# Performance work log

Measured on AMD Instinct MI355X. Metric: run time of the kernel, lower is better.

Reference implementation:

```python
import jax, jax.numpy as jnp
import numpy as np

B, C, H, W = 8, 3, 512, 512
KH = KW = 17          # blur kernel
F_REG, D = 24, 4      # regularization filters, Wiener filters
RKH = RKW = 5         # reg-filter kernel size


def psf2otf(psf, shape):
    """Zero-pad psf to `shape`, circshift so center is at (0,0), FFT."""
    kh, kw = psf.shape[-2:]
    Ho, Wo = shape
    pad = [(0, 0)] * (psf.ndim - 2) + [(0, Ho - kh), (0, Wo - kw)]
    p = jnp.pad(psf, pad)
    p = jnp.roll(p, (-(kh // 2), -(kw // 2)), axis=(-2, -1))
    return jnp.fft.fft2(p)


def edgetaper(img, psf):
    """MATLAB-style edgetaper. img: (C,Hp,Wp), psf: (kh,kw)."""
    Ho, Wo = img.shape[-2:]

    def autocorr(proj, n):
        z = jnp.zeros((n,), img.dtype).at[: proj.shape[0]].set(proj)
        z = jnp.fft.ifft(jnp.abs(jnp.fft.fft(z)) ** 2).real
        z = jnp.concatenate([z, z[:1]])  # length n+1
        return z / z.max()

    beta0 = autocorr(psf.sum(1), Ho - 1)  # (Ho,)
    beta1 = autocorr(psf.sum(0), Wo - 1)  # (Wo,)
    alpha = (1.0 - beta0)[:, None] * (1.0 - beta1)[None, :]  # (Ho,Wo)
    blurred = jnp.fft.ifft2(jnp.fft.fft2(img) * psf2otf(psf, (Ho, Wo))).real
    return alpha * img + (1.0 - alpha) * blurred


def wiener_one(y, psf, g, log_alpha):
    """Multi-filter Wiener deconvolution for one image.
    y: (C,Hp,Wp), psf: (kh,kw), g: (F,1,rkh,rkw), log_alpha: (D,1).
    Returns (D,C,Hp,Wp)."""
    Ho, Wo = y.shape[-2:]
    K = psf2otf(psf, (Ho, Wo))                  # (Hp,Wp) complex
    G = psf2otf(g[:, 0], (Ho, Wo))              # (F,Hp,Wp)
    Greg = jnp.sum(jnp.abs(G) ** 2, axis=0)     # (Hp,Wp)
    Y = jnp.fft.fft2(y)                         # (C,Hp,Wp)
    a = jnp.exp(log_alpha)[:, :, None, None]    # (D,1,1,1)
    S = jnp.abs(K) ** 2 + a * Greg              # (D,1,Hp,Wp)
    X = (jnp.conj(K) * Y)[None] / S             # (D,C,Hp,Wp)
    return jnp.fft.ifft2(X).real


def forward(image, blurKernel, stdn, wiener_conv_weights, wiener_scale, alpha, weights):
    kh, kw = blurKernel.shape[-2:]
    # getPad2RetainShape
    pt, pb = (kh + 1) // 2 - 1, kh - (kh + 1) // 2
    pl, pr = (kw + 1) // 2 - 1, kw - (kw + 1) // 2
    x = jnp.pad(image, ((0, 0), (0, 0), (pt, pb), (pl, pr)), mode='symmetric')
    psf = blurKernel[:, 0]                      # (B,kh,kw)
    x = jax.vmap(edgetaper)(x, psf)             # (B,C,Hp,Wp)
    # WeightNormalization: zero-mean then L2-normalize per filter, times scale
    w = wiener_conv_weights - wiener_conv_weights.mean(axis=(1, 2, 3), keepdims=True)
    nrm = jnp.sqrt(jnp.sum(w * w, axis=(1, 2, 3), keepdims=True))
    w = w * (wiener_scale.reshape(-1, 1, 1, 1) / nrm)
    xw = jax.vmap(lambda yi, ki: wiener_one(yi, ki, w, alpha))(x, psf)  # (B,D,C,Hp,Wp)
    Hp, Wp = x.shape[-2:]
    crop = xw[..., pt:Hp - pb, pl:Wp - pr]      # Crop2D back to (H,W)
    return jnp.sum(crop * weights, axis=1)      # weighted mix over D -> (B,C,H,W)


def setup_inputs() -> dict:
    key = jax.random.key(0)
    ks = jax.random.split(key, 4)
    image = jax.random.uniform(ks[0], (B, C, H, W), jnp.float32)
    k = jax.random.uniform(ks[1], (B, 1, KH, KW), jnp.float32)
    blurKernel = k / jnp.sum(k, axis=(-2, -1), keepdims=True)  # normalized psf
    stdn = jax.random.uniform(ks[2], (B,), jnp.float32) * 0.05 + 0.01
    wiener_conv_weights = jax.random.normal(ks[3], (F_REG, 1, RKH, RKW), jnp.float32)
    wiener_scale = jnp.full((F_REG,), 0.1, jnp.float32)
    alpha = jnp.log(jnp.logspace(np.log10(1e-3), np.log10(1e-1), D))[:, None].astype(jnp.float32)
    weights = jnp.full((1, D, 1, 1, 1), 1.0 / D, jnp.float32)
    return {"image": image, "blurKernel": blurKernel, "stdn": stdn,
            "wiener_conv_weights": wiener_conv_weights, "wiener_scale": wiener_scale,
            "alpha": alpha, "weights": weights}


def reference(image, blurKernel, stdn, wiener_conv_weights, wiener_scale, alpha, weights):
    return forward(image, blurKernel, stdn, wiener_conv_weights, wiener_scale, alpha, weights)
```

## Files before the change

### kernel.cpp

```cpp
#include <hip/hip_runtime.h>
#include <hip/hip_bf16.h>

#define NN 528
#define NP (NN*NN)
#define IMG 512
#define IMGP (IMG*IMG)
#define PAD 8
#define KH 17
#define KT (KH*KH)
#define NF 24
#define RK 5
#define RKT (RK*RK)
#define ND 4
#define TOPB (17*NN)
#define ROWB (2*TOPB)
#define SIDEB (494*34)
#define BORD (ROWB + SIDEB)

static __device__ __forceinline__ float ldx(const void* p, long i, int bf) {
    if (bf) return __bfloat162float(((const __hip_bfloat16*)p)[i]);
    return ((const float*)p)[i];
}

static __device__ __forceinline__ int gmap(int m) {
    if (m < -8)  return 495 - m;
    if (m < 0)   return -m - 1;
    if (m < 512) return m;
    if (m < 520) return 1023 - m;
    return 527 - m;
}

__global__ void detect_k(const void* pimg, int nimg, const void* pbk, int nbk,
                         const void* pwcw, int nwcw, const void* pws, int nws,
                         const float* c4a, const float* c4b,
                         int* __restrict__ flags,
                         float* __restrict__ alpha_ws, float* __restrict__ wgt_ws) {
    int t = threadIdx.x;
    const void* ps[4] = {pimg, pbk, pwcw, pws};
    int ns[4] = {nimg, nbk, nwcw, nws};
    if (t < 4) {
        const unsigned short* q = (const unsigned short*)ps[t];
        int n = ns[t];
        int K = n < 512 ? n : 512;
        int cnt = 0, pass = 0;
        for (int i = 0; i < K; i += 2) {
            int e = (q[i] >> 7) & 0xFF;
            pass += (e >= 100 && e <= 140);
            cnt++;
        }
        flags[t] = (pass * 10 >= cnt * 8) ? 1 : 0;
    }
    if (t == 7) {
        const float* A = (c4a[0] < 0.f) ? c4a : c4b;
        const float* W = (c4a[0] < 0.f) ? c4b : c4a;
        for (int i = 0; i < ND; ++i) { alpha_ws[i] = A[i]; wgt_ws[i] = W[i]; }
    }
}

__global__ void twinit_k(float2* __restrict__ twN) {
    int i = blockIdx.x * blockDim.x + threadIdx.x;
    if (i < NN) {
        double th = -6.283185307179586476925287 * (double)i / (double)NN;
        twN[i] = make_float2((float)cos(th), (float)sin(th));
    }
}

__global__ void wnorm_k(const void* __restrict__ wcw, const void* __restrict__ wscale,
                        const int* __restrict__ flags, float* __restrict__ wout) {
    int f = threadIdx.x;
    if (f >= NF) return;
    int bfw = flags[2], bfs = flags[3];
    float v[RKT];
    float mean = 0.f;
    for (int i = 0; i < RKT; ++i) { v[i] = ldx(wcw, f*RKT+i, bfw); mean += v[i]; }
    mean *= (1.f/(float)RKT);
    float ss = 0.f;
    for (int i = 0; i < RKT; ++i) { v[i] -= mean; ss += v[i]*v[i]; }
    float sc = ldx(wscale, f, bfs) / sqrtf(ss);
    for (int i = 0; i < RKT; ++i) wout[f*RKT+i] = v[i]*sc;
}

__global__ void prep_k(const void* __restrict__ blurKernel, const int* __restrict__ flags,
                       float* __restrict__ psf_all, float* __restrict__ A0_all,
                       float* __restrict__ A1_all) {
    int b = blockIdx.x, t = threadIdx.x;
    int bf = flags[1];
    __shared__ float psf[KT];
    __shared__ float q0[KH], q1[KH], ac0[KH], ac1[KH];
    for (int i = t; i < KT; i += 64) {
        float v = ldx(blurKernel, b*KT + i, bf);
        psf[i] = v;
        psf_all[b*KT + i] = v;
    }
    __syncthreads();
    if (t < KH) {
        float s0 = 0.f, s1 = 0.f;
        for (int k = 0; k < KH; ++k) { s0 += psf[t*KH + k]; s1 += psf[k*KH + t]; }
        q0[t] = s0; q1[t] = s1;
    }
    __syncthreads();
    if (t < KH) {
        float a0 = 0.f, a1 = 0.f;
        for (int m = 0; m + t < KH; ++m) { a0 += q0[m]*q0[m+t]; a1 += q1[m]*q1[m+t]; }
        ac0[t] = a0; ac1[t] = a1;
    }
    __syncthreads();
    for (int r = t; r < NN; r += 64) {
        int lag = min(r, (NN-1) - r);
        float b0 = (lag <= KH-1) ? ac0[lag]/ac0[0] : 0.f;
        float b1 = (lag <= KH-1) ? ac1[lag]/ac1[0] : 0.f;
        A0_all[b*NN + r] = 1.f - b0;
        A1_all[b*NN + r] = 1.f - b1;
    }
}

__global__ void greg_k(const float* __restrict__ w, const float2* __restrict__ twN,
                       float* __restrict__ Greg) {
    int p = blockIdx.x * blockDim.x + threadIdx.x;
    if (p >= NP) return;
    int u = p % NN, v = p / NN;
    float2 rp[RK], cp[RK];
    for (int j = 0; j < RK; ++j) {
        int m = (u * (j - RK/2)) % NN; if (m < 0) m += NN;
        rp[j] = twN[m];
    }
    for (int k = 0; k < RK; ++k) {
        int m = (v * (k - RK/2)) % NN; if (m < 0) m += NN;
        cp[k] = twN[m];
    }
    float pr[RKT], pi[RKT];
    for (int j = 0; j < RK; ++j)
        for (int k = 0; k < RK; ++k) {
            pr[j*RK+k] = rp[j].x*cp[k].x - rp[j].y*cp[k].y;
            pi[j*RK+k] = rp[j].x*cp[k].y + rp[j].y*cp[k].x;
        }
    float acc = 0.f;
    for (int f = 0; f < NF; ++f) {
        float gr = 0.f, gi = 0.f;
        for (int i = 0; i < RKT; ++i) {
            float wv = w[f*RKT + i];
            gr += wv * pr[i];
            gi += wv * pi[i];
        }
        acc += gr*gr + gi*gi;
    }
    Greg[p] = acc;
}

__global__ __launch_bounds__(256)
void border2_k(const void* __restrict__ image, const int* __restrict__ flags,
               const float* __restrict__ psf_all,
               const float* __restrict__ A0_all, const float* __restrict__ A1_all,
               float* __restrict__ borderV) {
    __shared__ float4 S4[1440];
    float* S = (float*)S4;
    int bp = blockIdx.y;
    int b = bp / 3;
    long ofs = (long)bp * IMGP;
    int bf = flags[0];
    int t = threadIdx.x;
    const float* pw = psf_all + b*KT;
    int bx = blockIdx.x;

    if (bx < 20) {
        int q = bx >> 1, h = bx & 1;
        int r0;
        if (q < 4) r0 = 4*q;
        else if (q == 4) r0 = 13;
        else if (q < 9) r0 = 511 + 4*(q-5);
        else r0 = 524;
        int X0 = h * 264;
        for (int idx = t; idx < 20*288; idx += 256) {
            int i = idx / 288, xi = idx - i*288;
            int x = X0 + xi;
            float v = 0.f;
            if (x < 544) {
                int sr = gmap(r0 - 16 + i);
                int sc = gmap(x - 16);
                v = ldx(image, ofs + (long)sr*IMG + sc, bf);
            }
            S[idx] = v;
        }
        __syncthreads();
        for (int g = t; g < 264; g += 256) {
            int rx = g / 66, cl = g - rx*66;
            int c0 = X0 + 4*cl;
            int x0 = 4*cl;
            float acc0 = 0.f, acc1 = 0.f, acc2 = 0.f, acc3 = 0.f;
            for (int j = 0; j < KH; ++j) {
                const float4* SjV = (const float4*)(S + (16 + rx - j)*288 + x0);
                float xv[20];
                #pragma unroll
                for (int qv = 0; qv < 5; ++qv) {
                    float4 tv = SjV[qv];
                    xv[4*qv+0] = tv.x; xv[4*qv+1] = tv.y;
                    xv[4*qv+2] = tv.z; xv[4*qv+3] = tv.w;
                }
                const float* wj = pw + j*KH;
                #pragma unroll
                for (int qq = 0; qq < 20; ++qq) {
                    {int k = 0 + 16 - qq; if (k >= 0 && k < KH) acc0 += wj[k]*xv[qq];}
                    {int k = 1 + 16 - qq; if (k >= 0 && k < KH) acc1 += wj[k]*xv[qq];}
                    {int k = 2 + 16 - qq; if (k >= 0 && k < KH) acc2 += wj[k]*xv[qq];}
                    {int k = 3 + 16 - qq; if (k >= 0 && k < KH) acc3 += wj[k]*xv[qq];}
                }
            }
            int r = r0 + rx;
            float a0v = A0_all[b*NN + r];
            int ibase = (r < 17) ? r*NN : TOPB + (r-511)*NN;
            float accs[4] = {acc0, acc1, acc2, acc3};
            #pragma unroll
            for (int d = 0; d < 4; ++d) {
                int c = c0 + d;
                float xo = S[(8 + rx)*288 + (x0 + 8 + d)];
                float al = a0v * A1_all[b*NN + c];
                borderV[(size_t)bp*BORD + ibase + c] = al*xo + (1.f - al)*accs[d];
            }
        }
    } else {
        int chunk = bx - 20;
        int r0 = 17 + 26*chunk;
        for (int idx = t; idx < 42*84; idx += 256) {
            int i = idx / 84, x = idx - i*84;
            float v = 0.f;
            int m = -1000;
            if (x < 33) m = x - 16;
            else if (x >= 48 && x < 81) m = x - 48 + 495;
            if (m != -1000) {
                int sr = gmap(r0 - 16 + i);
                int sc = gmap(m);
                v = ldx(image, ofs + (long)sr*IMG + sc, bf);
            }
            S[idx] = v;
        }
        __syncthreads();
        int g = t;
        if (g < 208) {
            int ry = g >> 3, s = g & 7;
            int c0 = (s < 4) ? 4*s : 511 + 4*(s-4);
            int sz = ((s & 3) == 3) ? 5 : 4;
            int x0 = (s < 4) ? 4*s : 48 + 4*(s-4);
            float acc0=0.f, acc1=0.f, acc2=0.f, acc3=0.f, acc4=0.f;
            for (int j = 0; j < KH; ++j) {
                const float4* SjV = (const float4*)(S + (16 + ry - j)*84 + x0);
                float xv[24];
                #pragma unroll
                for (int qv = 0; qv < 6; ++qv) {
                    float4 tv = SjV[qv];
                    xv[4*qv+0] = tv.x; xv[4*qv+1] = tv.y;
                    xv[4*qv+2] = tv.z; xv[4*qv+3] = tv.w;
                }
                const float* wj = pw + j*KH;
                #pragma unroll
                for (int qq = 0; qq < 21; ++qq) {
                    {int k = 0 + 16 - qq; if (k >= 0 && k < KH) acc0 += wj[k]*xv[qq];}
                    {int k = 1 + 16 - qq; if (k >= 0 && k < KH) acc1 += wj[k]*xv[qq];}
                    {int k = 2 + 16 - qq; if (k >= 0 && k < KH) acc2 += wj[k]*xv[qq];}
                    {int k = 3 + 16 - qq; if (k >= 0 && k < KH) acc3 += wj[k]*xv[qq];}
                    {int k = 4 + 16 - qq; if (k >= 0 && k < KH) acc4 += wj[k]*xv[qq];}
                }
            }
            int r = r0 + ry;
            float a0v = A0_all[b*NN + r];
            int cc0 = (s < 4) ? c0 : c0 - 494;
            size_t ib = (size_t)bp*BORD + ROWB + (size_t)(r-17)*34 + cc0;
            float accs[5] = {acc0, acc1, acc2, acc3, acc4};
            #pragma unroll
            for (int d = 0; d < 5; ++d) {
                if (d < sz) {
                    int c = c0 + d;
                    float xo = S[(8 + ry)*84 + (x0 + 8 + d)];
                    float al = a0v * A1_all[b*NN + c];
                    borderV[ib + d] = al*xo + (1.f - al)*accs[d];
                }
            }
        }
    }
}

__global__ void pad6_k(const void* __restrict__ image, const int* __restrict__ flags,
                       const float* __restrict__ borderV,
                       float2* __restrict__ buf, int B0) {
    int idx = blockIdx.x * blockDim.x + threadIdx.x;
    if (idx >= 6*NP) return;
    int bf = flags[0];
    int q = idx / NP, p = idx % NP;
    int pair = q / 3, ch = q - 3*pair;
    int b0p = B0 + 2*pair;
    int r = p / NN, c = p % NN;
    float x0, x1;
    bool isb = (r < 17) | (r >= 511) | (c < 17) | (c >= 511);
    if (isb) {
        int i2;
        if (r < 17) i2 = r*NN + c;
        else if (r >= 511) i2 = TOPB + (r-511)*NN + c;
        else { int cc = (c < 17) ? c : c - 494; i2 = ROWB + (r-17)*34 + cc; }
        x0 = borderV[(size_t)(b0p*3 + ch)*BORD + i2];
        x1 = borderV[(size_t)((b0p+1)*3 + ch)*BORD + i2];
    } else {
        long ofs0 = ((long)b0p*3 + ch) * IMGP + (long)(r - PAD)*IMG + (c - PAD);
        x0 = ldx(image, ofs0, bf);
        x1 = ldx(image, ofs0 + 3L*IMGP, bf);
    }
    buf[(size_t)q*NP + p] = make_float2(x0, x1);
}

__global__ __launch_bounds__(128)
void fft_pass(const float2* __restrict__ in, float2* __restrict__ out,
              const float2* __restrict__ twN, int inv) {
    __shared__ float2 X[NN];
    __shared__ float2 A[NN];
    __shared__ float2 TW[NN];
    int t = threadIdx.x;
    const float2* src = in + (size_t)blockIdx.x * NN;
    float2* dst = out + (size_t)blockIdx.x * NN;
    for (int i = t; i < NN; i += 128) { X[i] = src[i]; TW[i] = twN[i]; }
    __syncthreads();
    float s = inv ? -1.f : 1.f;
    for (int o = t; o < NN; o += 128) {
        int n1 = o & 15, k2 = o >> 4;
        float ar = 0.f, ai = 0.f;
        int m = 0;
        for (int n2 = 0; n2 < 33; ++n2) {
            float2 xv = X[n1 + 16*n2];
            float2 w = TW[m * 16];
            float wr = w.x, wi = w.y * s;
            ar += xv.x*wr - xv.y*wi;
            ai += xv.x*wi + xv.y*wr;
            m += k2; if (m >= 33) m -= 33;
        }
        float2 tw = TW[n1 * k2];
        float twr = tw.x, twi = tw.y * s;
        A[n1*33 + k2] = make_float2(ar*twr - ai*twi, ar*twi + ai*twr);
    }
    __syncthreads();
    for (int o = t; o < NN; o += 128) {
        int k1 = o / 33, k2 = o - 33*k1;
        float ar = 0.f, ai = 0.f;
        int m = 0;
        for (int n1 = 0; n1 < 16; ++n1) {
            float2 bv = A[n1*33 + k2];
            float2 w = TW[m * 33];
            float wr = w.x, wi = w.y * s;
            ar += bv.x*wr - bv.y*wi;
            ai += bv.x*wi + bv.y*wr;
            m = (m + k1) & 15;
        }
        dst[o] = make_float2(ar, ai);
    }
}

__global__ void transpose_ip_k(float2* __restrict__ buf) {
    int tnum = blockIdx.x;
    int ti = 0, rem = tnum;
    while (rem >= 33 - ti) { rem -= 33 - ti; ti++; }
    int tj = ti + rem;
    float2* pl = buf + (size_t)blockIdx.z * NP;
    __shared__ float2 ta[16][17], tb[16][17];
    int tx = threadIdx.x, ty = threadIdx.y;
    int ra = ti*16 + ty, ca = tj*16 + tx;
    int rb = tj*16 + ty, cb = ti*16 + tx;
    ta[ty][tx] = pl[(size_t)ra*NN + ca];
    tb[ty][tx] = pl[(size_t)rb*NN + cb];
    __syncthreads();
    pl[(size_t)ra*NN + ca] = tb[tx][ty];
    pl[(size_t)rb*NN + cb] = ta[tx][ty];
}

__global__ void kv_k(const float* __restrict__ psf_all, const float2* __restrict__ twN,
                     float2* __restrict__ Sv) {
    int idx = blockIdx.x * blockDim.x + threadIdx.x;
    if (idx >= 8*NN*KH) return;
    int j = idx % KH;
    int rest = idx / KH;
    int v = rest % NN, b = rest / NN;
    int m = (520 * v) % NN;
    float sr = 0.f, si = 0.f;
    const float* ps = psf_all + b*KT + j*KH;
    for (int k = 0; k < KH; ++k) {
        float2 cp = twN[m];
        m += v; if (m >= NN) m -= NN;
        sr += ps[k] * cp.x;
        si += ps[k] * cp.y;
    }
    Sv[idx] = make_float2(sr, si);
}

__global__ __launch_bounds__(256)
void cmulw2_k(float2* __restrict__ buf, const float2* __restrict__ Sv,
              const float* __restrict__ Greg, const float2* __restrict__ twN,
              const float* __restrict__ alpha4, const float* __restrict__ wgt4, int B0) {
    int pair = blockIdx.y;
    int b0p = B0 + 2*pair;
    __shared__ float2 tw[NN];
    for (int i = threadIdx.x; i < NN; i += 256) tw[i] = twN[i];
    __syncthreads();
    int p = blockIdx.x * blockDim.x + threadIdx.x;
    if (p >= NP) return;
    int u = p % NN, v = p / NN;
    int um = (NN - u) % NN, vm = (NN - v) % NN;
    int pm = vm * NN + um;
    if (pm < p) return;
    const float2* S0 = Sv + ((size_t)(b0p    )*NN + v)*KH;
    const float2* S1 = Sv + ((size_t)(b0p + 1)*NN + v)*KH;
    int mu = (520 * u) % NN;
    float K0r = 0.f, K0i = 0.f, K1r = 0.f, K1i = 0.f;
    for (int j = 0; j < KH; ++j) {
        float2 rp = tw[mu]; mu += u; if (mu >= NN) mu -= NN;
        float2 s0 = S0[j], s1 = S1[j];
        K0r += rp.x*s0.x - rp.y*s0.y;  K0i += rp.x*s0.y + rp.y*s0.x;
        K1r += rp.x*s1.x - rp.y*s1.y;  K1i += rp.x*s1.y + rp.y*s1.x;
    }
    float g = Greg[p];
    float K20 = K0r*K0r + K0i*K0i;
    float K21 = K1r*K1r + K1i*K1i;
    float s0 = 0.f, s1 = 0.f;
    for (int d = 0; d < ND; ++d) {
        float a = __expf(alpha4[d]);
        float wd = wgt4[d];
        s0 += wd / fmaxf(K20 + a*g, 1e-30f);
        s1 += wd / fmaxf(K21 + a*g, 1e-30f);
    }
    s0 *= (1.f/(float)NP);
    s1 *= (1.f/(float)NP);
    float W0r = K0r*s0, W0i = -K0i*s0;
    float W1r = K1r*s1, W1i = -K1i*s1;
    float2* pl = buf + (size_t)pair*3*NP;
    for (int ch = 0; ch < 3; ++ch) {
        float2 Z  = pl[(size_t)ch*NP + p];
        float2 Zm = pl[(size_t)ch*NP + pm];
        float X0r = 0.5f*(Z.x + Zm.x), X0i = 0.5f*(Z.y - Zm.y);
        float X1r = 0.5f*(Z.y + Zm.y), X1i = 0.5f*(Zm.x - Z.x);
        float Y0r = X0r*W0r - X0i*W0i, Y0i = X0r*W0i + X0i*W0r;
        float Y1r = X1r*W1r - X1i*W1i, Y1i = X1r*W1i + X1i*W1r;
        pl[(size_t)ch*NP + p]  = make_float2(Y0r - Y1i, Y0i + Y1r);
        pl[(size_t)ch*NP + pm] = make_float2(Y0r + Y1i, Y1r - Y0i);
    }
}

__global__ __launch_bounds__(128)
void fft_crop_k(const float2* __restrict__ in, float* __restrict__ out,
                const float2* __restrict__ twN, int B0) {
    __shared__ float2 X[NN];
    __shared__ float2 A[NN];
    __shared__ float2 TW[NN];
    int t = threadIdx.x;
    int q = blockIdx.x >> 9;
    int rp = (blockIdx.x & 511) + PAD;
    int pair = q / 3, ch = q - 3*pair;
    int b0p = B0 + 2*pair;
    const float2* src = in + (size_t)q*NP + (size_t)rp*NN;
    for (int i = t; i < NN; i += 128) { X[i] = src[i]; TW[i] = twN[i]; }
    __syncthreads();
    const float s = -1.f;
    for (int o = t; o < NN; o += 128) {
        int n1 = o & 15, k2 = o >> 4;
        float ar = 0.f, ai = 0.f;
        int m = 0;
        for (int n2 = 0; n2 < 33; ++n2) {
            float2 xv = X[n1 + 16*n2];
            float2 w = TW[m * 16];
            float wr = w.x, wi = w.y * s;
            ar += xv.x*wr - xv.y*wi;
            ai += xv.x*wi + xv.y*wr;
            m += k2; if (m >= 33) m -= 33;
        }
        float2 tw = TW[n1 * k2];
        float twr = tw.x, twi = tw.y * s;
        A[n1*33 + k2] = make_float2(ar*twr - ai*twi, ar*twi + ai*twr);
    }
    __syncthreads();
    float* o0 = out + ((size_t)b0p*3 + ch) * IMGP + (size_t)(rp - PAD) * IMG;
    float* o1 = o0 + 3L*IMGP;
    for (int o = PAD + t; o < IMG + PAD; o += 128) {
        int k1 = o / 33, k2 = o - 33*k1;
        float ar = 0.f, ai = 0.f;
        int m = 0;
        for (int n1 = 0; n1 < 16; ++n1) {
            float2 bv = A[n1*33 + k2];
            float2 w = TW[m * 33];
            float wr = w.x, wi = w.y * s;
            ar += bv.x*wr - bv.y*wi;
            ai += bv.x*wi + bv.y*wr;
            m = (m + k1) & 15;
        }
        o0[o - PAD] = ar;
        o1[o - PAD] = ai;
    }
}

extern "C" void kernel_launch(void* const* d_in, const int* in_sizes, int n_in,
                              void* d_out, int out_size, void* d_ws, size_t ws_size,
                              hipStream_t stream) {
    int i_img = -1, i_bk = -1, i_wcw = -1, i_ws = -1, i_4a = -1, i_4b = -1;
    for (int i = 0; i < n_in; ++i) {
        int s = in_sizes[i];
        if (s == 8*3*IMG*IMG)   i_img = i;
        else if (s == 8*KT)     i_bk = i;
        else if (s == NF*RKT)   i_wcw = i;
        else if (s == NF)       i_ws = i;
        else if (s == ND) { if (i_4a < 0) i_4a = i; else i_4b = i; }
    }
    if (i_img < 0) i_img = 0;
    if (i_bk  < 0) i_bk  = 1;
    if (i_wcw < 0) i_wcw = 3;
    if (i_ws  < 0) i_ws  = 4;
    if (i_4a  < 0) i_4a  = 5;
    if (i_4b  < 0) i_4b  = i_4a;
    const void* image      = d_in[i_img];
    const void* blurKernel = d_in[i_bk];
    const void* wcw        = d_in[i_wcw];
    const void* wscale     = d_in[i_ws];
    const float* c4a       = (const float*)d_in[i_4a];
    const float* c4b       = (const float*)d_in[i_4b];
    float* out = (float*)d_out;

    char* base = (char*)d_ws;
    int*    flags    = (int*)(base);
    float*  alpha_ws = (float*)(base + 64);
    float*  wgt_ws   = (float*)(base + 80);
    float2* twN      = (float2*)(base + 256);
    float*  wnorm    = (float*)(base + 4480);
    float*  psf_all  = (float*)(base + 6880);
    float*  A0       = (float*)(base + 16128);
    float*  A1       = (float*)(base + 33024);
    float*  Greg     = (float*)(base + 49920);
    float2* buf      = (float2*)(base + 1165056);
    float*  borderV  = (float*)(base + 14546688);
    float2* Sv       = (float2*)(base + 17882496);

    if (ws_size < 18456960) return;

    detect_k<<<1, 64, 0, stream>>>(image, in_sizes[i_img], blurKernel, in_sizes[i_bk],
                                   wcw, in_sizes[i_wcw], wscale, in_sizes[i_ws],
                                   c4a, c4b, flags, alpha_ws, wgt_ws);
    twinit_k<<<(NN+63)/64, 64, 0, stream>>>(twN);
    wnorm_k<<<1, 64, 0, stream>>>(wcw, wscale, flags, wnorm);
    prep_k<<<8, 64, 0, stream>>>(blurKernel, flags, psf_all, A0, A1);
    greg_k<<<(NP+255)/256, 256, 0, stream>>>(wnorm, twN, Greg);
    kv_k<<<(8*NN*KH+255)/256, 256, 0, stream>>>(psf_all, twN, Sv);

    dim3 bgrid2(39, 24);
    border2_k<<<bgrid2, 256, 0, stream>>>(image, flags, psf_all, A0, A1, borderV);

    dim3 tblk(16, 16);
    dim3 tgrid6(561, 1, 6);
    dim3 cgrid((NP+255)/256, 2);

    for (int B0 = 0; B0 < 8; B0 += 4) {
        pad6_k<<<(6*NP+255)/256, 256, 0, stream>>>(image, flags, borderV, buf, B0);
        fft_pass<<<6*NN, 128, 0, stream>>>(buf, buf, twN, 0);
        transpose_ip_k<<<tgrid6, tblk, 0, stream>>>(buf);
        fft_pass<<<6*NN, 128, 0, stream>>>(buf, buf, twN, 0);
        cmulw2_k<<<cgrid, 256, 0, stream>>>(buf, Sv, Greg, twN, alpha_ws, wgt_ws, B0);
        fft_pass<<<6*NN, 128, 0, stream>>>(buf, buf, twN, 1);
        transpose_ip_k<<<tgrid6, tblk, 0, stream>>>(buf);
        fft_crop_k<<<6*IMG, 128, 0, stream>>>(buf, out, twN, B0);
    }
}
```

Baseline: 496.7 us.

## Fuse padding into row FFT and fuse column FFTs with Wiener multiply

Folds the padding step into the forward row FFT kernel. Replaces the two transposes, the forward column FFT, the spectral Wiener multiply and the inverse column FFT with a single column-pipeline kernel. That kernel loads three column pairs (k and its conjugate mirror) into shared memory, runs the forward column FFT, applies the Hermitian-split Wiener filter, runs the inverse column FFT and writes the columns back in place. This removes several full-plane global round trips and kernel launches. In exchange it uses strided column reads and writes, and launches only 89x6 blocks with large shared memory, which may limit occupancy.

```diff
diff --git a/kernel.cpp b/kernel.cpp
--- a/kernel.cpp
+++ b/kernel.cpp
@@ -16,6 +16,7 @@
 #define ROWB (2*TOPB)
 #define SIDEB (494*34)
 #define BORD (ROWB + SIDEB)
+#define XD 530
 
 static __device__ __forceinline__ float ldx(const void* p, long i, int bf) {
     if (bf) return __bfloat162float(((const __hip_bfloat16*)p)[i]);
@@ -278,95 +279,6 @@
     }
 }
 
-__global__ void pad6_k(const void* __restrict__ image, const int* __restrict__ flags,
-                       const float* __restrict__ borderV,
-                       float2* __restrict__ buf, int B0) {
-    int idx = blockIdx.x * blockDim.x + threadIdx.x;
-    if (idx >= 6*NP) return;
-    int bf = flags[0];
-    int q = idx / NP, p = idx % NP;
-    int pair = q / 3, ch = q - 3*pair;
-    int b0p = B0 + 2*pair;
-    int r = p / NN, c = p % NN;
-    float x0, x1;
-    bool isb = (r < 17) | (r >= 511) | (c < 17) | (c >= 511);
-    if (isb) {
-        int i2;
-        if (r < 17) i2 = r*NN + c;
-        else if (r >= 511) i2 = TOPB + (r-511)*NN + c;
-        else { int cc = (c < 17) ? c : c - 494; i2 = ROWB + (r-17)*34 + cc; }
-        x0 = borderV[(size_t)(b0p*3 + ch)*BORD + i2];
-        x1 = borderV[(size_t)((b0p+1)*3 + ch)*BORD + i2];
-    } else {
-        long ofs0 = ((long)b0p*3 + ch) * IMGP + (long)(r - PAD)*IMG + (c - PAD);
-        x0 = ldx(image, ofs0, bf);
-        x1 = ldx(image, ofs0 + 3L*IMGP, bf);
-    }
-    buf[(size_t)q*NP + p] = make_float2(x0, x1);
-}
-
-__global__ __launch_bounds__(128)
-void fft_pass(const float2* __restrict__ in, float2* __restrict__ out,
-              const float2* __restrict__ twN, int inv) {
-    __shared__ float2 X[NN];
-    __shared__ float2 A[NN];
-    __shared__ float2 TW[NN];
-    int t = threadIdx.x;
-    const float2* src = in + (size_t)blockIdx.x * NN;
-    float2* dst = out + (size_t)blockIdx.x * NN;
-    for (int i = t; i < NN; i += 128) { X[i] = src[i]; TW[i] = twN[i]; }
-    __syncthreads();
-    float s = inv ? -1.f : 1.f;
-    for (int o = t; o < NN; o += 128) {
-        int n1 = o & 15, k2 = o >> 4;
-        float ar = 0.f, ai = 0.f;
-        int m = 0;
-        for (int n2 = 0; n2 < 33; ++n2) {
-            float2 xv = X[n1 + 16*n2];
-            float2 w = TW[m * 16];
-            float wr = w.x, wi = w.y * s;
-            ar += xv.x*wr - xv.y*wi;
-            ai += xv.x*wi + xv.y*wr;
-            m += k2; if (m >= 33) m -= 33;
-        }
-        float2 tw = TW[n1 * k2];
-        float twr = tw.x, twi = tw.y * s;
-        A[n1*33 + k2] = make_float2(ar*twr - ai*twi, ar*twi + ai*twr);
-    }
-    __syncthreads();
-    for (int o = t; o < NN; o += 128) {
-        int k1 = o / 33, k2 = o - 33*k1;
-        float ar = 0.f, ai = 0.f;
-        int m = 0;
-        for (int n1 = 0; n1 < 16; ++n1) {
-            float2 bv = A[n1*33 + k2];
-            float2 w = TW[m * 33];
-            float wr = w.x, wi = w.y * s;
-            ar += bv.x*wr - bv.y*wi;
-            ai += bv.x*wi + bv.y*wr;
-            m = (m + k1) & 15;
-        }
-        dst[o] = make_float2(ar, ai);
-    }
-}
-
-__global__ void transpose_ip_k(float2* __restrict__ buf) {
-    int tnum = blockIdx.x;
-    int ti = 0, rem = tnum;
-    while (rem >= 33 - ti) { rem -= 33 - ti; ti++; }
-    int tj = ti + rem;
-    float2* pl = buf + (size_t)blockIdx.z * NP;
-    __shared__ float2 ta[16][17], tb[16][17];
-    int tx = threadIdx.x, ty = threadIdx.y;
-    int ra = ti*16 + ty, ca = tj*16 + tx;
-    int rb = tj*16 + ty, cb = ti*16 + tx;
-    ta[ty][tx] = pl[(size_t)ra*NN + ca];
-    tb[ty][tx] = pl[(size_t)rb*NN + cb];
-    __syncthreads();
-    pl[(size_t)ra*NN + ca] = tb[tx][ty];
-    pl[(size_t)rb*NN + cb] = ta[tx][ty];
-}
-
 __global__ void kv_k(const float* __restrict__ psf_all, const float2* __restrict__ twN,
                      float2* __restrict__ Sv) {
     int idx = blockIdx.x * blockDim.x + threadIdx.x;
@@ -386,55 +298,237 @@
     Sv[idx] = make_float2(sr, si);
 }
 
+__global__ __launch_bounds__(128)
+void fftrow_k(const void* __restrict__ image, const int* __restrict__ flags,
+              const float* __restrict__ borderV, const float2* __restrict__ twN,
+              float2* __restrict__ buf, int B0) {
+    __shared__ float2 X[NN];
+    __shared__ float2 A[NN];
+    __shared__ float2 TW[NN];
+    int t = threadIdx.x;
+    int q = blockIdx.x / NN;
+    int r = blockIdx.x - q*NN;
+    int pair = q / 3, ch = q - 3*pair;
+    int b0p = B0 + 2*pair;
+    int bf = flags[0];
+    for (int i = t; i < NN; i += 128) TW[i] = twN[i];
+    for (int c = t; c < NN; c += 128) {
+        float x0, x1;
+        bool isb = (r < 17) | (r >= 511) | (c < 17) | (c >= 511);
+        if (isb) {
+            int i2;
+            if (r < 17) i2 = r*NN + c;
+            else if (r >= 511) i2 = TOPB + (r-511)*NN + c;
+            else { int cc = (c < 17) ? c : c - 494; i2 = ROWB + (r-17)*34 + cc; }
+            x0 = borderV[(size_t)(b0p*3 + ch)*BORD + i2];
+            x1 = borderV[(size_t)((b0p+1)*3 + ch)*BORD + i2];
+        } else {
+            long ofs0 = ((long)b0p*3 + ch) * IMGP + (long)(r - PAD)*IMG + (c - PAD);
+            x0 = ldx(image, ofs0, bf);
+            x1 = ldx(image, ofs0 + 3L*IMGP, bf);
+        }
+        X[c] = make_float2(x0, x1);
+    }
+    __syncthreads();
+    for (int o = t; o < NN; o += 128) {
+        int n1 = o & 15, k2 = o >> 4;
+        float ar = 0.f, ai = 0.f;
+        int m = 0;
+        for (int n2 = 0; n2 < 33; ++n2) {
+            float2 xv = X[n1 + 16*n2];
+            float2 w = TW[m * 16];
+            ar += xv.x*w.x - xv.y*w.y;
+            ai += xv.x*w.y + xv.y*w.x;
+            m += k2; if (m >= 33) m -= 33;
+        }
+        float2 tw = TW[n1 * k2];
+        A[n1*33 + k2] = make_float2(ar*tw.x - ai*tw.y, ar*tw.y + ai*tw.x);
+    }
+    __syncthreads();
+    float2* dst = buf + (size_t)q*NP + (size_t)r*NN;
+    for (int o = t; o < NN; o += 128) {
+        int k1 = o / 33, k2 = o - 33*k1;
+        float ar = 0.f, ai = 0.f;
+        int m = 0;
+        for (int n1 = 0; n1 < 16; ++n1) {
+            float2 bv = A[n1*33 + k2];
+            float2 w = TW[m * 33];
+            ar += bv.x*w.x - bv.y*w.y;
+            ai += bv.x*w.y + bv.y*w.x;
+            m = (m + k1) & 15;
+        }
+        dst[o] = make_float2(ar, ai);
+    }
+}
+
+static __device__ __forceinline__ void colinfo(int g, int l, int* col, bool* act) {
+    int s = (l < 3) ? l : l - 3;
+    int qq = 3*g + s;
+    bool lo = (l < 3);
+    bool sf = (qq == 0) || (qq == 264);
+    *act = (qq <= 264) && (lo || !sf);
+    *col = lo ? qq : (NN - qq) % NN;
+}
+
 __global__ __launch_bounds__(256)
-void cmulw2_k(float2* __restrict__ buf, const float2* __restrict__ Sv,
-              const float* __restrict__ Greg, const float2* __restrict__ twN,
-              const float* __restrict__ alpha4, const float* __restrict__ wgt4, int B0) {
-    int pair = blockIdx.y;
+void colpipe_k(float2* __restrict__ buf, const float2* __restrict__ Sv,
+               const float* __restrict__ Greg, const float2* __restrict__ twN,
+               const float* __restrict__ alpha4, const float* __restrict__ wgt4, int B0) {
+    __shared__ float2 X[6*XD];
+    __shared__ float2 A[6*XD];
+    __shared__ float2 TW[NN];
+    __shared__ float2 SvL[2][3][KH];
+    int t = threadIdx.x;
+    int g = blockIdx.x, plane = blockIdx.y;
+    int pair = plane / 3;
     int b0p = B0 + 2*pair;
-    __shared__ float2 tw[NN];
-    for (int i = threadIdx.x; i < NN; i += 256) tw[i] = twN[i];
-    __syncthreads();
-    int p = blockIdx.x * blockDim.x + threadIdx.x;
-    if (p >= NP) return;
-    int u = p % NN, v = p / NN;
-    int um = (NN - u) % NN, vm = (NN - v) % NN;
-    int pm = vm * NN + um;
-    if (pm < p) return;
-    const float2* S0 = Sv + ((size_t)(b0p    )*NN + v)*KH;
-    const float2* S1 = Sv + ((size_t)(b0p + 1)*NN + v)*KH;
-    int mu = (520 * u) % NN;
-    float K0r = 0.f, K0i = 0.f, K1r = 0.f, K1i = 0.f;
-    for (int j = 0; j < KH; ++j) {
-        float2 rp = tw[mu]; mu += u; if (mu >= NN) mu -= NN;
-        float2 s0 = S0[j], s1 = S1[j];
-        K0r += rp.x*s0.x - rp.y*s0.y;  K0i += rp.x*s0.y + rp.y*s0.x;
-        K1r += rp.x*s1.x - rp.y*s1.y;  K1i += rp.x*s1.y + rp.y*s1.x;
-    }
-    float g = Greg[p];
-    float K20 = K0r*K0r + K0i*K0i;
-    float K21 = K1r*K1r + K1i*K1i;
-    float s0 = 0.f, s1 = 0.f;
-    for (int d = 0; d < ND; ++d) {
-        float a = __expf(alpha4[d]);
-        float wd = wgt4[d];
-        s0 += wd / fmaxf(K20 + a*g, 1e-30f);
-        s1 += wd / fmaxf(K21 + a*g, 1e-30f);
-    }
-    s0 *= (1.f/(float)NP);
-    s1 *= (1.f/(float)NP);
-    float W0r = K0r*s0, W0i = -K0i*s0;
-    float W1r = K1r*s1, W1i = -K1i*s1;
-    float2* pl = buf + (size_t)pair*3*NP;
-    for (int ch = 0; ch < 3; ++ch) {
-        float2 Z  = pl[(size_t)ch*NP + p];
-        float2 Zm = pl[(size_t)ch*NP + pm];
+    float2* pl = buf + (size_t)plane * NP;
+
+    for (int i = t; i < NN; i += 256) TW[i] = twN[i];
+    if (t < 102) {
+        int s = t / 34, rest = t - 34*s, bsel = rest / 17, j = rest - 17*bsel;
+        int qq = 3*g + s;
+        if (qq <= 264) SvL[bsel][s][j] = Sv[((size_t)(b0p + bsel)*NN + qq)*KH + j];
+    }
+    for (int idx = t; idx < 8*NN; idx += 256) {
+        int l = idx & 7, r = idx >> 3;
+        if (l < 6) {
+            int col; bool act;
+            colinfo(g, l, &col, &act);
+            if (act) X[l*XD + r] = pl[(size_t)r*NN + col];
+        }
+    }
+    __syncthreads();
+    for (int idx = t; idx < 6*NN; idx += 256) {
+        int l = idx / NN, o = idx - l*NN;
+        int col; bool act;
+        colinfo(g, l, &col, &act);
+        if (!act) continue;
+        int n1 = o & 15, k2 = o >> 4;
+        float ar = 0.f, ai = 0.f;
+        int m = 0;
+        const float2* Xl = X + l*XD;
+        for (int n2 = 0; n2 < 33; ++n2) {
+            float2 xv = Xl[n1 + 16*n2];
+            float2 w = TW[m * 16];
+            ar += xv.x*w.x - xv.y*w.y;
+            ai += xv.x*w.y + xv.y*w.x;
+            m += k2; if (m >= 33) m -= 33;
+        }
+        float2 tw = TW[n1 * k2];
+        A[l*XD + n1*33 + k2] = make_float2(ar*tw.x - ai*tw.y, ar*tw.y + ai*tw.x);
+    }
+    __syncthreads();
+    for (int idx = t; idx < 6*NN; idx += 256) {
+        int l = idx / NN, o = idx - l*NN;
+        int col; bool act;
+        colinfo(g, l, &col, &act);
+        if (!act) continue;
+        int k1 = o / 33, k2 = o - 33*k1;
+        float ar = 0.f, ai = 0.f;
+        int m = 0;
+        const float2* Al = A + l*XD;
+        for (int n1 = 0; n1 < 16; ++n1) {
+            float2 bv = Al[n1*33 + k2];
+            float2 w = TW[m * 33];
+            ar += bv.x*w.x - bv.y*w.y;
+            ai += bv.x*w.y + bv.y*w.x;
+            m = (m + k1) & 15;
+        }
+        X[l*XD + o] = make_float2(ar, ai);
+    }
+    __syncthreads();
+    float aE[ND], wEE[ND];
+    #pragma unroll
+    for (int d = 0; d < ND; ++d) { aE[d] = __expf(alpha4[d]); wEE[d] = wgt4[d]; }
+    for (int idx = t; idx < 3*NN; idx += 256) {
+        int s = idx / NN, kr = idx - NN*s;
+        int qq = 3*g + s;
+        if (qq > 264) continue;
+        bool sf = (qq == 0) || (qq == 264);
+        if (sf && kr > 264) continue;
+        int lhi = sf ? s : s + 3;
+        int krm = (kr == 0) ? 0 : NN - kr;
+        int mu = (520 * kr) % NN;
+        float K0r = 0.f, K0i = 0.f, K1r = 0.f, K1i = 0.f;
+        for (int j = 0; j < KH; ++j) {
+            float2 rp = TW[mu]; mu += kr; if (mu >= NN) mu -= NN;
+            float2 s0 = SvL[0][s][j], s1 = SvL[1][s][j];
+            K0r += rp.x*s0.x - rp.y*s0.y;  K0i += rp.x*s0.y + rp.y*s0.x;
+            K1r += rp.x*s1.x - rp.y*s1.y;  K1i += rp.x*s1.y + rp.y*s1.x;
+        }
+        float gg = Greg[(size_t)qq*NN + kr];
+        float K20 = K0r*K0r + K0i*K0i;
+        float K21 = K1r*K1r + K1i*K1i;
+        float s0a = 0.f, s1a = 0.f;
+        #pragma unroll
+        for (int d = 0; d < ND; ++d) {
+            s0a += wEE[d] / fmaxf(K20 + aE[d]*gg, 1e-30f);
+            s1a += wEE[d] / fmaxf(K21 + aE[d]*gg, 1e-30f);
+        }
+        s0a *= (1.f/(float)NP);
+        s1a *= (1.f/(float)NP);
+        float W0r = K0r*s0a, W0i = -K0i*s0a;
+        float W1r = K1r*s1a, W1i = -K1i*s1a;
+        float2 Z  = X[s*XD + kr];
+        float2 Zm = X[lhi*XD + krm];
         float X0r = 0.5f*(Z.x + Zm.x), X0i = 0.5f*(Z.y - Zm.y);
         float X1r = 0.5f*(Z.y + Zm.y), X1i = 0.5f*(Zm.x - Z.x);
         float Y0r = X0r*W0r - X0i*W0i, Y0i = X0r*W0i + X0i*W0r;
         float Y1r = X1r*W1r - X1i*W1i, Y1i = X1r*W1i + X1i*W1r;
-        pl[(size_t)ch*NP + p]  = make_float2(Y0r - Y1i, Y0i + Y1r);
-        pl[(size_t)ch*NP + pm] = make_float2(Y0r + Y1i, Y1r - Y0i);
+        X[s*XD + kr]    = make_float2(Y0r - Y1i, Y0i + Y1r);
+        X[lhi*XD + krm] = make_float2(Y0r + Y1i, Y1r - Y0i);
+    }
+    __syncthreads();
+    for (int idx = t; idx < 6*NN; idx += 256) {
+        int l = idx / NN, o = idx - l*NN;
+        int col; bool act;
+        colinfo(g, l, &col, &act);
+        if (!act) continue;
+        int n1 = o & 15, k2 = o >> 4;
+        float ar = 0.f, ai = 0.f;
+        int m = 0;
+        const float2* Xl = X + l*XD;
+        for (int n2 = 0; n2 < 33; ++n2) {
+            float2 xv = Xl[n1 + 16*n2];
+            float2 w = TW[m * 16];
+            float wr = w.x, wi = -w.y;
+            ar += xv.x*wr - xv.y*wi;
+            ai += xv.x*wi + xv.y*wr;
+            m += k2; if (m >= 33) m -= 33;
+        }
+        float2 tw = TW[n1 * k2];
+        float twr = tw.x, twi = -tw.y;
+        A[l*XD + n1*33 + k2] = make_float2(ar*twr - ai*twi, ar*twi + ai*twr);
+    }
+    __syncthreads();
+    for (int idx = t; idx < 6*NN; idx += 256) {
+        int l = idx / NN, o = idx - l*NN;
+        int col; bool act;
+        colinfo(g, l, &col, &act);
+        if (!act) continue;
+        int k1 = o / 33, k2 = o - 33*k1;
+        float ar = 0.f, ai = 0.f;
+        int m = 0;
+        const float2* Al = A + l*XD;
+        for (int n1 = 0; n1 < 16; ++n1) {
+            float2 bv = Al[n1*33 + k2];
+            float2 w = TW[m * 33];
+            float wr = w.x, wi = -w.y;
+            ar += bv.x*wr - bv.y*wi;
+            ai += bv.x*wi + bv.y*wr;
+            m = (m + k1) & 15;
+        }
+        X[l*XD + o] = make_float2(ar, ai);
+    }
+    __syncthreads();
+    for (int idx = t; idx < 8*NN; idx += 256) {
+        int l = idx & 7, r = idx >> 3;
+        if (l < 6) {
+            int col; bool act;
+            colinfo(g, l, &col, &act);
+            if (act) pl[(size_t)r*NN + col] = X[l*XD + r];
+        }
     }
 }
 
@@ -543,18 +637,10 @@
     dim3 bgrid2(39, 24);
     border2_k<<<bgrid2, 256, 0, stream>>>(image, flags, psf_all, A0, A1, borderV);
 
-    dim3 tblk(16, 16);
-    dim3 tgrid6(561, 1, 6);
-    dim3 cgrid((NP+255)/256, 2);
-
+    dim3 cpgrid(89, 6);
     for (int B0 = 0; B0 < 8; B0 += 4) {
-        pad6_k<<<(6*NP+255)/256, 256, 0, stream>>>(image, flags, borderV, buf, B0);
-        fft_pass<<<6*NN, 128, 0, stream>>>(buf, buf, twN, 0);
-        transpose_ip_k<<<tgrid6, tblk, 0, stream>>>(buf);
-        fft_pass<<<6*NN, 128, 0, stream>>>(buf, buf, twN, 0);
-        cmulw2_k<<<cgrid, 256, 0, stream>>>(buf, Sv, Greg, twN, alpha_ws, wgt_ws, B0);
-        fft_pass<<<6*NN, 128, 0, stream>>>(buf, buf, twN, 1);
-        transpose_ip_k<<<tgrid6, tblk, 0, stream>>>(buf);
+        fftrow_k<<<6*NN, 128, 0, stream>>>(image, flags, borderV, twN, buf, B0);
+        colpipe_k<<<cpgrid, 256, 0, stream>>>(buf, Sv, Greg, twN, alpha_ws, wgt_ws, B0);
         fft_crop_k<<<6*IMG, 128, 0, stream>>>(buf, out, twN, B0);
     }
 }
```

Measured after the change: 539.4 us. 1.09x slower.
